# Optimization experiments

Measured on AMD Instinct MI355X. Metric: run time of the kernel, lower is better.

## Reference

```python
import jax, jax.numpy as jnp
import numpy as np

ALPHA = 0.2          # LeakyReLU negative slope
NEG_INF = -9.0e15    # padding value used by the torch code before softmax


def setup_inputs() -> dict:
    key = jax.random.key(0)
    k1, k2, k3, k4 = jax.random.split(key, 4)
    B, N, F_IN, F_OUT = 32, 1024, 128, 128
    # Dense 0/1 adjacency with self-loops (every node has degree >= 1)
    u = jax.random.uniform(k1, (B, N, N))
    adj = (u < 0.03).astype(jnp.float32)
    adj = jnp.maximum(adj, jnp.eye(N, dtype=jnp.float32)[None, :, :])
    batch_features = jax.random.normal(k2, (B, N, F_IN), dtype=jnp.float32)
    W = jax.random.normal(k3, (F_OUT, F_IN), dtype=jnp.float32) * 0.1  # nn.Linear weight [out,in]
    a = jax.random.normal(k4, (2 * F_OUT, 1), dtype=jnp.float32) * 0.1
    return {"batch_graphs": adj, "batch_features": batch_features, "W": W, "a": a}


def reference(batch_graphs, batch_features, W, a):
    # batch_graphs: [B,N,N] 0/1 adjacency; batch_features: [B,N,F_in]
    D = W.shape[0]
    h = jnp.einsum('bnf,df->bnd', batch_features, W)  # fc (no bias), dropout=0 is a no-op
    # score(i,j) = LeakyReLU(a[:D].h_i + a[D:].h_j); concat order is [center_i || neighbor_j]
    a_src = a[:D, 0]
    a_dst = a[D:, 0]
    s = h @ a_src                                   # [B,N] center term
    t = h @ a_dst                                   # [B,N] neighbor term
    scores = s[:, :, None] + t[:, None, :]          # [B,N,N]
    scores = jnp.where(scores > 0, scores, ALPHA * scores)
    # segmented softmax over each node's neighbors (pad_sequence with -9e15 == masked softmax)
    masked = jnp.where(batch_graphs == 1.0, scores, NEG_INF)
    attn = jax.nn.softmax(masked, axis=-1) * batch_graphs  # *adj zeros non-edges exactly (and deg-0 rows)
    # weighted sum of neighbor features scattered back to each node
    out = jnp.einsum('bij,bjd->bid', attn, h)       # [B,N,D]
    return out
```

## Files before the change

kernel.cpp:

```cpp
#include <hip/hip_runtime.h>
#include <hip/hip_bf16.h>

#define B_ 32
#define N_ 1024
#define F_ 128
#define ALPHA_ 0.2f
#define PSTR 72

typedef __attribute__((ext_vector_type(8))) short short8_t;
typedef __attribute__((ext_vector_type(4))) short short4_t;
typedef __attribute__((ext_vector_type(4))) float f32x4;

static __device__ __forceinline__ unsigned short bf16b(float f) {
    return __bfloat16_as_ushort(__float2bfloat16(f));
}

#define WAIT_LGKM() asm volatile("s_waitcnt lgkmcnt(0)" ::: "memory")
#define SCHEDB()    __builtin_amdgcn_sched_barrier(0)
#define BAR()       __builtin_amdgcn_s_barrier()

__global__ __launch_bounds__(256) void hst_kernel(
    const float* __restrict__ feat, const float* __restrict__ W,
    const float* __restrict__ a, unsigned short* __restrict__ hT,
    float* __restrict__ s_out, float* __restrict__ t_out)
{
    __shared__ unsigned short Wt[128 * 128];
    __shared__ float fl[64 * 128];
    const int tid = threadIdx.x;
    const long row0 = (long)blockIdx.x * 64;
    const int b  = (int)(row0 >> 10);
    const int jb = (int)(row0 & 1023);

    for (int i = tid; i < 128 * 128; i += 256) {
        int d = i >> 7, k = i & 127;
        Wt[k * 128 + d] = bf16b(W[i]);
    }
    for (int i = tid; i < 64 * 128; i += 256) {
        int r = i >> 7, k = i & 127;
        fl[r * 128 + ((k + 8 * (r >> 2)) & 127)] = feat[(row0 + r) * 128 + k];
    }
    __syncthreads();

    const int oct = tid & 15;
    const int rg  = tid >> 4;
    const int d0  = oct * 8;
    const int r0  = rg * 4;

    float acc[4][8];
    #pragma unroll
    for (int q = 0; q < 4; ++q)
        #pragma unroll
        for (int c = 0; c < 8; ++c) acc[q][c] = 0.f;

    for (int kc = 0; kc < 128; kc += 4) {
        float wv[4][8];
        #pragma unroll
        for (int kk = 0; kk < 4; ++kk) {
            short8_t wr = *reinterpret_cast<const short8_t*>(&Wt[(kc + kk) * 128 + d0]);
            #pragma unroll
            for (int c = 0; c < 8; ++c) {
                union { unsigned u; float f; } cv;
                cv.u = ((unsigned)(unsigned short)wr[c]) << 16;
                wv[kk][c] = cv.f;
            }
        }
        #pragma unroll
        for (int q = 0; q < 4; ++q) {
            int r = r0 + q;
            int koff = (kc + 8 * (r >> 2)) & 127;
            float4 fv = *reinterpret_cast<const float4*>(&fl[r * 128 + koff]);
            float fq[4] = {fv.x, fv.y, fv.z, fv.w};
            #pragma unroll
            for (int kk = 0; kk < 4; ++kk)
                #pragma unroll
                for (int c = 0; c < 8; ++c)
                    acc[q][c] = fmaf(fq[kk], wv[kk][c], acc[q][c]);
        }
    }

    float asrc[8], adst[8];
    #pragma unroll
    for (int c = 0; c < 8; ++c) { asrc[c] = a[d0 + c]; adst[c] = a[128 + d0 + c]; }
    #pragma unroll
    for (int q = 0; q < 4; ++q) {
        long row = row0 + r0 + q;
        float sv = 0.f, tv = 0.f;
        #pragma unroll
        for (int c = 0; c < 8; ++c) {
            sv = fmaf(acc[q][c], asrc[c], sv);
            tv = fmaf(acc[q][c], adst[c], tv);
        }
        #pragma unroll
        for (int off = 1; off < 16; off <<= 1) {
            sv += __shfl_xor(sv, off);
            tv += __shfl_xor(tv, off);
        }
        if (oct == 0) { s_out[row] = sv; t_out[row] = tv; }
    }

    __syncthreads();
    #pragma unroll
    for (int q = 0; q < 4; ++q) {
        int r = r0 + q;
        int base0 = (d0 + 4 * rg) & 127;
        int base1 = (d0 + 4 + 4 * rg) & 127;
        *reinterpret_cast<float4*>(&fl[r * 128 + base0]) =
            make_float4(acc[q][0], acc[q][1], acc[q][2], acc[q][3]);
        *reinterpret_cast<float4*>(&fl[r * 128 + base1]) =
            make_float4(acc[q][4], acc[q][5], acc[q][6], acc[q][7]);
    }
    __syncthreads();

    {
        const int d    = tid >> 1;
        const int half = tid & 1;
        unsigned short* dst = hT + ((size_t)b * F_ + d) * N_ + jb + half * 32;
        #pragma unroll
        for (int qq = 0; qq < 4; ++qq) {
            short8_t pk;
            #pragma unroll
            for (int e = 0; e < 8; ++e) {
                int j = half * 32 + qq * 8 + e;
                pk[e] = (short)bf16b(fl[j * 128 + ((d + 4 * (j >> 2)) & 127)]);
            }
            *reinterpret_cast<short8_t*>(dst + qq * 8) = pk;
        }
    }
}

__global__ __launch_bounds__(512, 4) void attn5_kernel(
    const float* __restrict__ adj, const unsigned short* __restrict__ hT,
    const float* __restrict__ s_in, const float* __restrict__ t_in,
    float* __restrict__ out)
{
    __shared__ unsigned short ht[128 * PSTR];
    __shared__ unsigned short pt[64 * PSTR];
    __shared__ float tl[N_];
    __shared__ float sl[64], rsl[64];

    const int tid = threadIdx.x;
    const int w   = tid >> 6;

    const int blk = (blockIdx.x & 7) * 64 + (blockIdx.x >> 3);
    const int b   = blk >> 4;
    const int i0  = (blk & 15) * 64;

    tl[tid]       = t_in[b * N_ + tid];
    tl[tid + 512] = t_in[b * N_ + tid + 512];
    if (tid < 64) sl[tid] = s_in[b * N_ + i0 + tid];

    const int gi = tid >> 3;
    const int gj = (tid & 7) * 8;
    const float* arow = adj + ((size_t)(b * N_ + i0 + gi)) * N_ + gj;

    const unsigned short* hTb = hT + (size_t)b * F_ * N_;

    float4   a_reg[2][2];
    short8_t h_reg[2][2];
#define LOAD_A(K) do {                                                         \
    a_reg[(K) & 1][0] = *reinterpret_cast<const float4*>(arow + (K) * 64);     \
    a_reg[(K) & 1][1] = *reinterpret_cast<const float4*>(arow + (K) * 64 + 4); \
} while (0)
#define LOAD_H(K) do {                                                         \
    _Pragma("unroll")                                                          \
    for (int c = 0; c < 2; ++c) {                                              \
        int ch = tid + c * 512;                                                \
        h_reg[(K) & 1][c] = *reinterpret_cast<const short8_t*>(                \
            hTb + (size_t)(ch >> 3) * N_ + ((K) * 64 + (ch & 7) * 8));         \
    }                                                                          \
} while (0)

    const int m0 = (w >> 2) * 32;
    const int n0 = (w & 3) * 32;
    const int lm = tid & 15;
    const int kg = (tid & 63) >> 4;

    f32x4 acc[2][2];
    #pragma unroll
    for (int nf = 0; nf < 2; ++nf)
        #pragma unroll
        for (int mf = 0; mf < 2; ++mf) acc[nf][mf] = (f32x4){0.f, 0.f, 0.f, 0.f};
    float rs = 0.f;

    LOAD_A(0);
    LOAD_H(0);
    WAIT_LGKM();
    SCHEDB();
    BAR();
    const float s_i = sl[gi];

    #pragma unroll
    for (int k = 0; k < 16; ++k) {
        if (k + 1 < 16) { LOAD_A(k + 1); LOAD_H(k + 1); }
        #pragma unroll
        for (int c = 0; c < 2; ++c) {
            int ch = tid + c * 512;
            *reinterpret_cast<short8_t*>(&ht[(ch >> 3) * PSTR + (ch & 7) * 8]) =
                h_reg[k & 1][c];
        }
        {
            float4 a0 = a_reg[k & 1][0];
            float4 a1 = a_reg[k & 1][1];
            float4 t0 = *reinterpret_cast<const float4*>(&tl[k * 64 + gj]);
            float4 t1 = *reinterpret_cast<const float4*>(&tl[k * 64 + gj + 4]);
            short4_t pk0, pk1;
            #pragma unroll
            for (int e = 0; e < 4; ++e) {
                float sc0 = s_i + (&t0.x)[e];
                sc0 = fmaxf(sc0, ALPHA_ * sc0);
                float p = __expf(sc0) * (&a0.x)[e];
                rs += p;
                pk0[e] = (short)bf16b(p);
            }
            #pragma unroll
            for (int e = 0; e < 4; ++e) {
                float sc1 = s_i + (&t1.x)[e];
                sc1 = fmaxf(sc1, ALPHA_ * sc1);
                float p = __expf(sc1) * (&a1.x)[e];
                rs += p;
                pk1[e] = (short)bf16b(p);
            }
            *reinterpret_cast<short4_t*>(&pt[gi * PSTR + gj])     = pk0;
            *reinterpret_cast<short4_t*>(&pt[gi * PSTR + gj + 4]) = pk1;
        }
        WAIT_LGKM();
        SCHEDB();
        BAR();
        #pragma unroll
        for (int ks = 0; ks < 2; ++ks) {
            short8_t b0 = *reinterpret_cast<const short8_t*>(
                &ht[(n0 + lm) * PSTR + ks * 32 + kg * 8]);
            short8_t b1 = *reinterpret_cast<const short8_t*>(
                &ht[(n0 + 16 + lm) * PSTR + ks * 32 + kg * 8]);
            short8_t a0f = *reinterpret_cast<const short8_t*>(
                &pt[(m0 + lm) * PSTR + ks * 32 + kg * 8]);
            short8_t a1f = *reinterpret_cast<const short8_t*>(
                &pt[(m0 + 16 + lm) * PSTR + ks * 32 + kg * 8]);
            acc[0][0] = __builtin_amdgcn_mfma_f32_16x16x32_bf16(a0f, b0, acc[0][0], 0, 0, 0);
            acc[1][0] = __builtin_amdgcn_mfma_f32_16x16x32_bf16(a0f, b1, acc[1][0], 0, 0, 0);
            acc[0][1] = __builtin_amdgcn_mfma_f32_16x16x32_bf16(a1f, b0, acc[0][1], 0, 0, 0);
            acc[1][1] = __builtin_amdgcn_mfma_f32_16x16x32_bf16(a1f, b1, acc[1][1], 0, 0, 0);
        }
        BAR();
    }

    rs += __shfl_xor(rs, 1);
    rs += __shfl_xor(rs, 2);
    rs += __shfl_xor(rs, 4);
    if ((tid & 7) == 0) rsl[gi] = 1.0f / rs;
    __syncthreads();

    const int rbase = m0 + ((tid & 63) >> 4) * 4;
    float* ob = out + ((size_t)(b * N_ + i0)) * F_;
    #pragma unroll
    for (int mf = 0; mf < 2; ++mf) {
        f32x4 inv = *reinterpret_cast<const f32x4*>(&rsl[rbase + mf * 16]);
        #pragma unroll
        for (int r = 0; r < 4; ++r) {
            int row = rbase + mf * 16 + r;
            #pragma unroll
            for (int nf = 0; nf < 2; ++nf)
                ob[(size_t)row * F_ + n0 + nf * 16 + lm] = acc[nf][mf][r] * inv[r];
        }
    }
#undef LOAD_A
#undef LOAD_H
}

extern "C" void kernel_launch(void* const* d_in, const int* in_sizes, int n_in,
                              void* d_out, int out_size, void* d_ws, size_t ws_size,
                              hipStream_t stream)
{
    const float* adj  = (const float*)d_in[0];
    const float* feat = (const float*)d_in[1];
    const float* W    = (const float*)d_in[2];
    const float* a    = (const float*)d_in[3];
    float* out = (float*)d_out;

    unsigned short* hT = (unsigned short*)d_ws;
    float* s = (float*)((char*)d_ws + (size_t)B_ * F_ * N_ * 2);
    float* t = s + (size_t)B_ * N_;

    hst_kernel<<<(B_ * N_) / 64, 256, 0, stream>>>(feat, W, a, hT, s, t);
    attn5_kernel<<<B_ * 16, 512, 0, stream>>>(adj, hT, s, t, out);
}
```

Baseline: 62.30 us.

## Fuse projection and attention kernels into one cooperative launch with grid sync

Merges the feature projection (h, s, t computation) and the masked-softmax attention aggregation into a single cooperative kernel, separated by a grid-wide barrier. Each block computes its 64-row slice of h, writes transposed bf16 h and s/t to workspace, syncs the grid, then runs the MFMA attention loop. Adjacency prefetch is issued before the projection phase to overlap with it. This removes one kernel launch and lets the adjacency loads start early, at the cost of a grid sync and a requirement that all 512 blocks be co-resident, with the two-kernel path kept as a fallback.

```diff
diff --git a/kernel.cpp b/kernel.cpp
--- a/kernel.cpp
+++ b/kernel.cpp
@@ -1,5 +1,6 @@
 #include <hip/hip_runtime.h>
 #include <hip/hip_bf16.h>
+#include <hip/hip_cooperative_groups.h>
 
 #define B_ 32
 #define N_ 1024
@@ -7,6 +8,8 @@
 #define ALPHA_ 0.2f
 #define PSTR 72
 
+namespace cg = cooperative_groups;
+
 typedef __attribute__((ext_vector_type(8))) short short8_t;
 typedef __attribute__((ext_vector_type(4))) short short4_t;
 typedef __attribute__((ext_vector_type(4))) float f32x4;
@@ -14,10 +17,262 @@
 static __device__ __forceinline__ unsigned short bf16b(float f) {
     return __bfloat16_as_ushort(__float2bfloat16(f));
 }
+static __device__ __forceinline__ float bf2f(unsigned short u) {
+    union { unsigned u; float f; } cv; cv.u = ((unsigned)u) << 16; return cv.f;
+}
 
 #define WAIT_LGKM() asm volatile("s_waitcnt lgkmcnt(0)" ::: "memory")
 #define SCHEDB()    __builtin_amdgcn_sched_barrier(0)
 #define BAR()       __builtin_amdgcn_s_barrier()
+
+__global__ __launch_bounds__(512, 4) void fused_kernel(
+    const float* __restrict__ feat, const float* __restrict__ W,
+    const float* __restrict__ a,    const float* __restrict__ adj,
+    unsigned short* __restrict__ hT, float* __restrict__ s_g,
+    float* __restrict__ t_g, float* __restrict__ out)
+{
+    __shared__ __align__(16) char smem[49152];
+    unsigned short* Wt  = (unsigned short*)smem;
+    unsigned short* flb = (unsigned short*)(smem + 32768);
+    unsigned short* ht  = (unsigned short*)smem;
+    unsigned short* pt  = (unsigned short*)(smem + 18432);
+    float*          tl  = (float*)(smem + 27648);
+    float*          sl  = (float*)(smem + 31744);
+    float*          rsl = (float*)(smem + 32000);
+
+    const int tid = threadIdx.x;
+    const int blk = ((int)blockIdx.x & 7) * 64 + ((int)blockIdx.x >> 3);
+    const int b   = blk >> 4;
+    const int i0  = (blk & 15) * 64;
+    const long row0 = (long)blk * 64;
+
+    const int gi = tid >> 3;
+    const int gj = (tid & 7) * 8;
+    const float* arow = adj + ((size_t)(b * N_ + i0 + gi)) * N_ + gj;
+    float4 a_reg[2][2];
+#define LOAD_A(K) do {                                                         \
+    a_reg[(K) & 1][0] = *reinterpret_cast<const float4*>(arow + (K) * 64);     \
+    a_reg[(K) & 1][1] = *reinterpret_cast<const float4*>(arow + (K) * 64 + 4); \
+} while (0)
+
+    for (int i = tid; i < 128 * 128; i += 512) {
+        int d = i >> 7, k = i & 127;
+        Wt[k * 128 + d] = bf16b(W[i]);
+    }
+    for (int i = tid; i < 64 * 128; i += 512) {
+        int r = i >> 7, k = i & 127;
+        flb[r * 128 + ((k + 8 * (r >> 2)) & 127)] = bf16b(feat[(row0 + r) * 128 + k]);
+    }
+    __syncthreads();
+
+    LOAD_A(0);
+    LOAD_A(1);
+
+    const int oct = tid & 15;
+    const int rg  = tid >> 4;
+    const int d0  = oct * 8;
+    const int r0  = rg * 2;
+
+    float acc1[2][8];
+    #pragma unroll
+    for (int q = 0; q < 2; ++q)
+        #pragma unroll
+        for (int c = 0; c < 8; ++c) acc1[q][c] = 0.f;
+
+    for (int kc = 0; kc < 128; kc += 4) {
+        float wv[4][8];
+        #pragma unroll
+        for (int kk = 0; kk < 4; ++kk) {
+            short8_t wr = *reinterpret_cast<const short8_t*>(&Wt[(kc + kk) * 128 + d0]);
+            #pragma unroll
+            for (int c = 0; c < 8; ++c) wv[kk][c] = bf2f((unsigned short)wr[c]);
+        }
+        #pragma unroll
+        for (int q = 0; q < 2; ++q) {
+            int r = r0 + q;
+            int koff = (kc + 8 * (r >> 2)) & 127;
+            short4_t fv = *reinterpret_cast<const short4_t*>(&flb[r * 128 + koff]);
+            float fq[4];
+            #pragma unroll
+            for (int e = 0; e < 4; ++e) fq[e] = bf2f((unsigned short)fv[e]);
+            #pragma unroll
+            for (int kk = 0; kk < 4; ++kk)
+                #pragma unroll
+                for (int c = 0; c < 8; ++c)
+                    acc1[q][c] = fmaf(fq[kk], wv[kk][c], acc1[q][c]);
+        }
+    }
+
+    {
+        float asrc[8], adst[8];
+        #pragma unroll
+        for (int c = 0; c < 8; ++c) { asrc[c] = a[d0 + c]; adst[c] = a[128 + d0 + c]; }
+        #pragma unroll
+        for (int q = 0; q < 2; ++q) {
+            long row = row0 + r0 + q;
+            float sv = 0.f, tv = 0.f;
+            #pragma unroll
+            for (int c = 0; c < 8; ++c) {
+                sv = fmaf(acc1[q][c], asrc[c], sv);
+                tv = fmaf(acc1[q][c], adst[c], tv);
+            }
+            #pragma unroll
+            for (int off = 1; off < 16; off <<= 1) {
+                sv += __shfl_xor(sv, off);
+                tv += __shfl_xor(tv, off);
+            }
+            if (oct == 0) { s_g[row] = sv; t_g[row] = tv; }
+        }
+    }
+
+    __syncthreads();
+    #pragma unroll
+    for (int q = 0; q < 2; ++q) {
+        int r = r0 + q;
+        int base0 = (d0 + 4 * (r >> 2)) & 127;
+        int base1 = (d0 + 4 + 4 * (r >> 2)) & 127;
+        short4_t p0, p1;
+        #pragma unroll
+        for (int e = 0; e < 4; ++e) {
+            p0[e] = (short)bf16b(acc1[q][e]);
+            p1[e] = (short)bf16b(acc1[q][4 + e]);
+        }
+        *reinterpret_cast<short4_t*>(&flb[r * 128 + base0]) = p0;
+        *reinterpret_cast<short4_t*>(&flb[r * 128 + base1]) = p1;
+    }
+    __syncthreads();
+
+    {
+        const int d  = tid >> 2;
+        const int qg = tid & 3;
+        unsigned short* dst = hT + ((size_t)b * F_ + d) * N_ + i0 + qg * 16;
+        #pragma unroll
+        for (int qq = 0; qq < 2; ++qq) {
+            short8_t pk;
+            #pragma unroll
+            for (int e = 0; e < 8; ++e) {
+                int j = qg * 16 + qq * 8 + e;
+                pk[e] = (short)flb[j * 128 + ((d + 4 * (j >> 2)) & 127)];
+            }
+            *reinterpret_cast<short8_t*>(dst + qq * 8) = pk;
+        }
+    }
+
+    __threadfence();
+    cg::this_grid().sync();
+
+    tl[tid]       = t_g[b * N_ + tid];
+    tl[tid + 512] = t_g[b * N_ + tid + 512];
+    if (tid < 64) sl[tid] = s_g[b * N_ + i0 + tid];
+
+    const unsigned short* hTb = hT + (size_t)b * F_ * N_;
+    short8_t h_reg[2][2];
+#define LOAD_H(K) do {                                                         \
+    _Pragma("unroll")                                                          \
+    for (int c = 0; c < 2; ++c) {                                              \
+        int ch = tid + c * 512;                                                \
+        h_reg[(K) & 1][c] = *reinterpret_cast<const short8_t*>(                \
+            hTb + (size_t)(ch >> 3) * N_ + ((K) * 64 + (ch & 7) * 8));         \
+    }                                                                          \
+} while (0)
+
+    const int w  = tid >> 6;
+    const int m0 = (w >> 2) * 32;
+    const int n0 = (w & 3) * 32;
+    const int lm = tid & 15;
+    const int kg = (tid & 63) >> 4;
+
+    f32x4 acc[2][2];
+    #pragma unroll
+    for (int nf = 0; nf < 2; ++nf)
+        #pragma unroll
+        for (int mf = 0; mf < 2; ++mf) acc[nf][mf] = (f32x4){0.f, 0.f, 0.f, 0.f};
+    float rs = 0.f;
+
+    LOAD_H(0);
+    WAIT_LGKM();
+    SCHEDB();
+    BAR();
+    const float s_i = sl[gi];
+
+    #pragma unroll
+    for (int k = 0; k < 16; ++k) {
+        if (k + 1 < 16) LOAD_H(k + 1);
+        #pragma unroll
+        for (int c = 0; c < 2; ++c) {
+            int ch = tid + c * 512;
+            *reinterpret_cast<short8_t*>(&ht[(ch >> 3) * PSTR + (ch & 7) * 8]) =
+                h_reg[k & 1][c];
+        }
+        {
+            float4 a0 = a_reg[k & 1][0];
+            float4 a1 = a_reg[k & 1][1];
+            float4 t0 = *reinterpret_cast<const float4*>(&tl[k * 64 + gj]);
+            float4 t1 = *reinterpret_cast<const float4*>(&tl[k * 64 + gj + 4]);
+            short4_t pk0, pk1;
+            #pragma unroll
+            for (int e = 0; e < 4; ++e) {
+                float sc0 = s_i + (&t0.x)[e];
+                sc0 = fmaxf(sc0, ALPHA_ * sc0);
+                float p = __expf(sc0) * (&a0.x)[e];
+                rs += p;
+                pk0[e] = (short)bf16b(p);
+            }
+            #pragma unroll
+            for (int e = 0; e < 4; ++e) {
+                float sc1 = s_i + (&t1.x)[e];
+                sc1 = fmaxf(sc1, ALPHA_ * sc1);
+                float p = __expf(sc1) * (&a1.x)[e];
+                rs += p;
+                pk1[e] = (short)bf16b(p);
+            }
+            *reinterpret_cast<short4_t*>(&pt[gi * PSTR + gj])     = pk0;
+            *reinterpret_cast<short4_t*>(&pt[gi * PSTR + gj + 4]) = pk1;
+        }
+        if (k + 2 < 16) LOAD_A(k + 2);
+        WAIT_LGKM();
+        SCHEDB();
+        BAR();
+        #pragma unroll
+        for (int ks = 0; ks < 2; ++ks) {
+            short8_t b0 = *reinterpret_cast<const short8_t*>(
+                &ht[(n0 + lm) * PSTR + ks * 32 + kg * 8]);
+            short8_t b1 = *reinterpret_cast<const short8_t*>(
+                &ht[(n0 + 16 + lm) * PSTR + ks * 32 + kg * 8]);
+            short8_t a0f = *reinterpret_cast<const short8_t*>(
+                &pt[(m0 + lm) * PSTR + ks * 32 + kg * 8]);
+            short8_t a1f = *reinterpret_cast<const short8_t*>(
+                &pt[(m0 + 16 + lm) * PSTR + ks * 32 + kg * 8]);
+            acc[0][0] = __builtin_amdgcn_mfma_f32_16x16x32_bf16(a0f, b0, acc[0][0], 0, 0, 0);
+            acc[1][0] = __builtin_amdgcn_mfma_f32_16x16x32_bf16(a0f, b1, acc[1][0], 0, 0, 0);
+            acc[0][1] = __builtin_amdgcn_mfma_f32_16x16x32_bf16(a1f, b0, acc[0][1], 0, 0, 0);
+            acc[1][1] = __builtin_amdgcn_mfma_f32_16x16x32_bf16(a1f, b1, acc[1][1], 0, 0, 0);
+        }
+        BAR();
+    }
+
+    rs += __shfl_xor(rs, 1);
+    rs += __shfl_xor(rs, 2);
+    rs += __shfl_xor(rs, 4);
+    if ((tid & 7) == 0) rsl[gi] = 1.0f / rs;
+    __syncthreads();
+
+    const int rbase = m0 + ((tid & 63) >> 4) * 4;
+    float* ob = out + ((size_t)(b * N_ + i0)) * F_;
+    #pragma unroll
+    for (int mf = 0; mf < 2; ++mf) {
+        f32x4 inv = *reinterpret_cast<const f32x4*>(&rsl[rbase + mf * 16]);
+        #pragma unroll
+        for (int r = 0; r < 4; ++r) {
+            int row = rbase + mf * 16 + r;
+            #pragma unroll
+            for (int nf = 0; nf < 2; ++nf)
+                ob[(size_t)row * F_ + n0 + nf * 16 + lm] = acc[nf][mf][r] * inv[r];
+        }
+    }
+#undef LOAD_A
+#undef LOAD_H
+}
 
 __global__ __launch_bounds__(256) void hst_kernel(
     const float* __restrict__ feat, const float* __restrict__ W,
@@ -58,11 +313,7 @@
         for (int kk = 0; kk < 4; ++kk) {
             short8_t wr = *reinterpret_cast<const short8_t*>(&Wt[(kc + kk) * 128 + d0]);
             #pragma unroll
-            for (int c = 0; c < 8; ++c) {
-                union { unsigned u; float f; } cv;
-                cv.u = ((unsigned)(unsigned short)wr[c]) << 16;
-                wv[kk][c] = cv.f;
-            }
+            for (int c = 0; c < 8; ++c) wv[kk][c] = bf2f((unsigned short)wr[c]);
         }
         #pragma unroll
         for (int q = 0; q < 4; ++q) {
@@ -281,6 +532,12 @@
     float* s = (float*)((char*)d_ws + (size_t)B_ * F_ * N_ * 2);
     float* t = s + (size_t)B_ * N_;
 
-    hst_kernel<<<(B_ * N_) / 64, 256, 0, stream>>>(feat, W, a, hT, s, t);
-    attn5_kernel<<<B_ * 16, 512, 0, stream>>>(adj, hT, s, t, out);
+    void* args[] = { (void*)&feat, (void*)&W, (void*)&a, (void*)&adj,
+                     (void*)&hT, (void*)&s, (void*)&t, (void*)&out };
+    hipError_t err = hipLaunchCooperativeKernel(
+        (const void*)fused_kernel, dim3(B_ * 16), dim3(512), args, 0, stream);
+    if (err != hipSuccess) {
+        hst_kernel<<<(B_ * N_) / 64, 256, 0, stream>>>(feat, W, a, hT, s, t);
+        attn5_kernel<<<B_ * 16, 512, 0, stream>>>(adj, hT, s, t, out);
+    }
 }
```

Measured after the change: 218.8 us. 251% more time.
